# Kernel optimization log

Measured on AMD Instinct MI355X. Metric: run time of the kernel, lower is better.

## Reference

```python
import jax, jax.numpy as jnp
import numpy as np

N = 100000        # nodes
E = 1600000       # edges
F_IN = 128        # input features
H = 64            # hidden
B = 256           # graphs in batch
MIN_SCORE = 1e-3  # SAGPooling min_score
TOL = 1e-7        # PyG topk tolerance
NEG = jnp.float32(-1e30)


def setup_inputs() -> dict:
    key = jax.random.key(0)
    ks = jax.random.split(key, 24)
    x = jax.random.normal(ks[0], (N, F_IN), jnp.float32)
    src = jax.random.randint(ks[1], (E,), 0, N, dtype=jnp.int32)
    dst = jax.random.randint(ks[2], (E,), 0, N, dtype=jnp.int32)
    batch = jnp.sort(jax.random.randint(ks[3], (N,), 0, B, dtype=jnp.int32))
    node_attention = jax.random.uniform(ks[4], (N,), jnp.float32)

    def lin(k, i, o):
        return jax.random.normal(k, (i, o), jnp.float32) / np.float32(np.sqrt(i))

    p = {
        'W11': lin(ks[5], F_IN, H), 'b11': jnp.zeros((H,), jnp.float32),
        'W12': lin(ks[6], H, H),    'b12': jnp.zeros((H,), jnp.float32),
        'gW1': lin(ks[7], H, 1),    'gb1': jnp.zeros((1,), jnp.float32),
        'W21': lin(ks[8], H, H),    'b21': jnp.zeros((H,), jnp.float32),
        'W22': lin(ks[9], H, H),    'b22': jnp.zeros((H,), jnp.float32),
        'gW2': lin(ks[10], H, 1),   'gb2': jnp.zeros((1,), jnp.float32),
        'W31': lin(ks[11], H, H),   'b31': jnp.zeros((H,), jnp.float32),
        'W32': lin(ks[12], H, H),   'b32': jnp.zeros((H,), jnp.float32),
        'Wl':  lin(ks[13], H, 1),   'bl': jnp.zeros((1,), jnp.float32),
    }
    return dict(x=x, src=src, dst=dst, batch=batch, node_attention=node_attention, **p)


def gin_conv(x, src, dst, emask, W1, b1, W2, b2):
    # GINConv, eps=0: mlp(x + sum_{j in N(i)} x_j), edges masked by emask
    agg = jax.ops.segment_sum(x[src] * emask[:, None], dst, num_segments=N)
    h = x + agg
    return jax.nn.relu(h @ W1 + b1) @ W2 + b2


def gcn_attn(x, src, dst, emask, nmask, W, b):
    # GCNConv(H,1) with self-loops + symmetric normalization on the masked graph
    h = x @ W  # [N,1]
    deg = jax.ops.segment_sum(emask, dst, num_segments=N) + nmask
    dinv = jnp.where(deg > 0, jax.lax.rsqrt(jnp.maximum(deg, 1e-12)), 0.0)
    coef = dinv[src] * dinv[dst] * emask
    out = jax.ops.segment_sum(h[src] * coef[:, None], dst, num_segments=N)
    out = out + h * (dinv * dinv * nmask)[:, None] + b
    return out[:, 0]


def seg_softmax(a, batch, nmask):
    am = jnp.where(nmask > 0, a, NEG)
    m = jax.ops.segment_max(am, batch, num_segments=B)
    e = jnp.where(nmask > 0, jnp.exp(a - m[batch]), 0.0)
    s = jax.ops.segment_sum(e, batch, num_segments=B)
    return e / jnp.maximum(s[batch], 1e-30)


def sag_pool(x, src, dst, emask, nmask, batch, W, b):
    attn = gcn_attn(x, src, dst, emask, nmask, W, b)
    score = seg_softmax(attn, batch, nmask)
    smax = jax.ops.segment_max(jnp.where(nmask > 0, score, NEG), batch, num_segments=B)
    thr = jnp.minimum(MIN_SCORE, smax[batch] - TOL)
    keep = ((nmask > 0) & (score > thr)).astype(x.dtype)
    x2 = x * (score * keep)[:, None]          # x[perm] * score[perm], masked form
    emask2 = emask * keep[src] * keep[dst]    # filter_adj
    return x2, emask2, keep, score


def reference(x, src, dst, batch, node_attention,
              W11, b11, W12, b12, gW1, gb1,
              W21, b21, W22, b22, gW2, gb2,
              W31, b31, W32, b32, Wl, bl):
    emask = jnp.ones((E,), x.dtype)
    nmask0 = jnp.ones((N,), x.dtype)

    h = jax.nn.relu(gin_conv(x, src, dst, emask, W11, b11, W12, b12))
    h, emask, keep1, _ = sag_pool(h, src, dst, emask, nmask0, batch, gW1, gb1)

    h = jax.nn.relu(gin_conv(h, src, dst, emask, W21, b21, W22, b22))
    h, emask, keep2, score2 = sag_pool(h, src, dst, emask, keep1, batch, gW2, gb2)

    ratio = jnp.sum(keep2) / jnp.float32(N)

    h = jax.nn.relu(gin_conv(h, src, dst, emask, W31, b31, W32, b32))

    # global max pool over surviving nodes
    hm = jnp.where(keep2[:, None] > 0, h, NEG)
    g = jax.ops.segment_max(hm, batch, num_segments=B)
    out = g @ Wl + bl  # [B,1]

    # attention KL loss; perm2 indexes the pool1-compacted array (as in the source)
    r1 = jnp.clip(jnp.cumsum(keep1).astype(jnp.int32) - 1, 0, N - 1)
    t = node_attention[r1]
    logp = jnp.log(score2 + 1e-14)
    kl = jnp.where(t > 0, t * jnp.log(jnp.maximum(t, 1e-38)), 0.0) - t * logp
    kl = kl * keep2
    s = jax.ops.segment_sum(kl, batch, num_segments=B)
    c = jax.ops.segment_sum(keep2, batch, num_segments=B)
    attn_loss = s / jnp.maximum(c, 1.0)  # scatter_mean

    return out, attn_loss, ratio
```

## Files before the change

### kernel.cpp

```cpp
#include <hip/hip_runtime.h>
#include <hip/hip_fp16.h>
#include <math.h>

#define NN 100000
#define NE 1600000
#define NB 256
#define NEGF (-1e30f)
#define NSCAN_BLK ((NN + 1023) / 1024)
#define GVB 1024
#define P_SORT 256
#define NBKT 391
#define HLEN (NBKT * P_SORT)
#define HSCAN_BLK ((HLEN + 1023) / 1024)
#define BKT_CAP 6144
#define NMASKW 1566

__global__ void k_hist_coarse(const int* __restrict__ dst, const int* __restrict__ batch,
                              int* __restrict__ offs, int* __restrict__ H) {
    __shared__ int lh[NBKT];
    int p = blockIdx.x, tid = threadIdx.x;
    if (p == 0) {
        for (int g = tid; g <= NB; g += 256) {
            int lo = 0, hi = NN;
            while (lo < hi) { int mid = (lo + hi) >> 1; if (batch[mid] < g) lo = mid + 1; else hi = mid; }
            offs[g] = lo;
        }
    }
    for (int i = tid; i < NBKT; i += 256) lh[i] = 0;
    __syncthreads();
    int c0 = p * (NE / P_SORT), c1 = c0 + NE / P_SORT;
    for (int i = c0 + tid; i < c1; i += 256) atomicAdd(&lh[dst[i] >> 8], 1);
    __syncthreads();
    for (int i = tid; i < NBKT; i += 256) H[i * P_SORT + p] = lh[i];
}
__global__ void k_iscan_blk(const int* __restrict__ in, int* __restrict__ pref,
                            int* __restrict__ bsums, int len) {
    int blk = blockIdx.x, tid = threadIdx.x;
    int base = blk * 1024;
    int vals[4], tsum = 0;
    for (int j = 0; j < 4; ++j) {
        int idx = base + tid * 4 + j;
        int v = (idx < len) ? in[idx] : 0;
        vals[j] = tsum; tsum += v;
    }
    __shared__ int sh[256];
    sh[tid] = tsum; __syncthreads();
    for (int o = 1; o < 256; o <<= 1) {
        int v = (tid >= o) ? sh[tid - o] : 0;
        __syncthreads();
        sh[tid] += v;
        __syncthreads();
    }
    int excl = sh[tid] - tsum;
    for (int j = 0; j < 4; ++j) {
        int idx = base + tid * 4 + j;
        if (idx < len) pref[idx] = excl + vals[j];
    }
    if (tid == 255) bsums[blk] = sh[255];
}
__global__ void k_iscan_add(int* __restrict__ pref, const int* __restrict__ bsums, int len) {
    __shared__ int sh[256];
    int t = threadIdx.x;
    int sb = blockIdx.x >> 2;
    sh[t] = (t < sb) ? bsums[t] : 0;
    __syncthreads();
    for (int o = 128; o > 0; o >>= 1) { if (t < o) sh[t] += sh[t + o]; __syncthreads(); }
    int pre = sh[0];
    int idx = blockIdx.x * 256 + t;
    if (idx < len) pref[idx] += pre;
}
__global__ void k_scatter_pairs(const int* __restrict__ src, const int* __restrict__ dst,
                                const int* __restrict__ Hs, int2* __restrict__ ebuf) {
    __shared__ int curs[NBKT];
    int p = blockIdx.x, tid = threadIdx.x;
    for (int i = tid; i < NBKT; i += 256) curs[i] = Hs[i * P_SORT + p];
    __syncthreads();
    int c0 = p * (NE / P_SORT), c1 = c0 + NE / P_SORT;
    for (int i = c0 + tid; i < c1; i += 256) {
        int d = dst[i];
        int pos = atomicAdd(&curs[d >> 8], 1);
        ebuf[pos] = make_int2(src[i], d);
    }
}
__global__ void k_bucket_csr(const int2* __restrict__ ebuf, const int* __restrict__ Hs,
                             int* __restrict__ roffs, int* __restrict__ csrc) {
    __shared__ int hist2[256];
    __shared__ int curs2[256];
    __shared__ int sh[256];
    __shared__ int stage[BKT_CAP];
    int b = blockIdx.x, tid = threadIdx.x;
    int e0 = Hs[b * P_SORT];
    int e1 = (b + 1 < NBKT) ? Hs[(b + 1) * P_SORT] : NE;
    int n0 = b * 256;
    int cntb = e1 - e0;
    if (b == 0 && tid == 0) roffs[NN] = NE;
    hist2[tid] = 0;
    __syncthreads();
    for (int i = e0 + tid; i < e1; i += 256) atomicAdd(&hist2[ebuf[i].y & 255], 1);
    __syncthreads();
    int v = hist2[tid];
    sh[tid] = v; __syncthreads();
    for (int o = 1; o < 256; o <<= 1) {
        int u = (tid >= o) ? sh[tid - o] : 0;
        __syncthreads();
        sh[tid] += u;
        __syncthreads();
    }
    int excl = sh[tid] - v;
    int node = n0 + tid;
    if (node < NN) roffs[node] = e0 + excl;
    curs2[tid] = excl;
    __syncthreads();
    if (cntb <= BKT_CAP) {
        for (int i = e0 + tid; i < e1; i += 256) {
            int2 pr = ebuf[i];
            int pos = atomicAdd(&curs2[pr.y & 255], 1);
            stage[pos] = pr.x;
        }
        __syncthreads();
        for (int i = tid; i < cntb; i += 256) csrc[e0 + i] = stage[i];
    } else {
        for (int i = e0 + tid; i < e1; i += 256) {
            int2 pr = ebuf[i];
            int pos = atomicAdd(&curs2[pr.y & 255], 1);
            csrc[e0 + pos] = pr.x;
        }
    }
}

__global__ __launch_bounds__(256) void k_pre1_g(const float* __restrict__ x,
                                                const float* __restrict__ W,
                                                float* __restrict__ y) {
    __shared__ float lds[4][4 * 128];
    int tid = threadIdx.x, w = tid >> 6, l = tid & 63;
    float Wc[128];
#pragma unroll
    for (int k = 0; k < 128; ++k) Wc[k] = W[k * 64 + l];
    float* row = lds[w];
    int g = blockIdx.x * 4 + w;
    const int G = GVB * 4;
    for (int t = g; t < NN / 4; t += G) {
        int n0 = t * 4;
#pragma unroll
        for (int r = 0; r < 4; ++r) {
            row[r * 128 + l]      = x[(size_t)(n0 + r) * 128 + l];
            row[r * 128 + 64 + l] = x[(size_t)(n0 + r) * 128 + 64 + l];
        }
        __builtin_amdgcn_wave_barrier();
        float acc[4] = {0.f, 0.f, 0.f, 0.f};
#pragma unroll
        for (int k = 0; k < 128; k += 4) {
#pragma unroll
            for (int r = 0; r < 4; ++r) {
                float4 bv = *(const float4*)&row[r * 128 + k];
                acc[r] = fmaf(bv.x, Wc[k],     acc[r]);
                acc[r] = fmaf(bv.y, Wc[k + 1], acc[r]);
                acc[r] = fmaf(bv.z, Wc[k + 2], acc[r]);
                acc[r] = fmaf(bv.w, Wc[k + 3], acc[r]);
            }
        }
        __builtin_amdgcn_wave_barrier();
#pragma unroll
        for (int r = 0; r < 4; ++r) y[(size_t)(n0 + r) * 64 + l] = acc[r];
    }
}

__global__ __launch_bounds__(256) void k_pre23_h(const float* __restrict__ h,
                                                 const float* __restrict__ sk,
                                                 const float* __restrict__ W,
                                                 __half* __restrict__ yh) {
    __shared__ float lds[4][8 * 64];
    int tid = threadIdx.x, w = tid >> 6, l = tid & 63;
    float Wc[64];
#pragma unroll
    for (int k = 0; k < 64; ++k) Wc[k] = W[k * 64 + l];
    float* row = lds[w];
    int g = blockIdx.x * 4 + w;
    const int G = GVB * 4;
    for (int t = g; t < NN / 8; t += G) {
        int n0 = t * 8;
#pragma unroll
        for (int r = 0; r < 8; ++r) row[r * 64 + l] = h[(size_t)(n0 + r) * 64 + l];
        __builtin_amdgcn_wave_barrier();
        float acc[8] = {0.f, 0.f, 0.f, 0.f, 0.f, 0.f, 0.f, 0.f};
#pragma unroll
        for (int k = 0; k < 64; k += 4) {
#pragma unroll
            for (int r = 0; r < 8; ++r) {
                float4 bv = *(const float4*)&row[r * 64 + k];
                acc[r] = fmaf(bv.x, Wc[k],     acc[r]);
                acc[r] = fmaf(bv.y, Wc[k + 1], acc[r]);
                acc[r] = fmaf(bv.z, Wc[k + 2], acc[r]);
                acc[r] = fmaf(bv.w, Wc[k + 3], acc[r]);
            }
        }
        __builtin_amdgcn_wave_barrier();
#pragma unroll
        for (int r = 0; r < 8; ++r)
            yh[(size_t)(n0 + r) * 64 + l] = __float2half(acc[r] * sk[n0 + r]);
    }
}

__global__ __launch_bounds__(256) void k_post_g(const float* __restrict__ zp,
                                                const float* __restrict__ W2,
                                                const float* __restrict__ b2,
                                                const float* __restrict__ gW,
                                                const int* __restrict__ roffs,
                                                const int* __restrict__ cnt,
                                                const float* __restrict__ keep,
                                                float* __restrict__ hOut,
                                                float* __restrict__ hwd,
                                                float* __restrict__ dinv, int mode) {
    __shared__ float lds[4][8 * 64];
    int tid = threadIdx.x, w = tid >> 6, l = tid & 63;
    float Wc[64];
#pragma unroll
    for (int k = 0; k < 64; ++k) Wc[k] = W2[k * 64 + l];
    float b2v = b2[l];
    float gWv = (mode < 3) ? gW[l] : 0.f;
    float* row = lds[w];
    int g = blockIdx.x * 4 + w;
    const int G = GVB * 4;
    for (int t = g; t < NN / 8; t += G) {
        int n0 = t * 8;
#pragma unroll
        for (int r = 0; r < 8; ++r) row[r * 64 + l] = zp[(size_t)(n0 + r) * 64 + l];
        __builtin_amdgcn_wave_barrier();
        float acc[8];
#pragma unroll
        for (int r = 0; r < 8; ++r) acc[r] = b2v;
#pragma unroll
        for (int k = 0; k < 64; k += 4) {
#pragma unroll
            for (int r = 0; r < 8; ++r) {
                float4 bv = *(const float4*)&row[r * 64 + k];
                acc[r] = fmaf(bv.x, Wc[k],     acc[r]);
                acc[r] = fmaf(bv.y, Wc[k + 1], acc[r]);
                acc[r] = fmaf(bv.z, Wc[k + 2], acc[r]);
                acc[r] = fmaf(bv.w, Wc[k + 3], acc[r]);
            }
        }
        __builtin_amdgcn_wave_barrier();
#pragma unroll
        for (int r = 0; r < 8; ++r) {
            acc[r] = fmaxf(acc[r], 0.f);
            hOut[(size_t)(n0 + r) * 64 + l] = acc[r];
        }
        if (mode < 3) {
#pragma unroll
            for (int r = 0; r < 8; ++r) {
                float t2 = acc[r] * gWv;
                for (int o = 32; o > 0; o >>= 1) t2 += __shfl_down(t2, o, 64);
                if (l == 0) {
                    int n = n0 + r;
                    float di;
                    if (mode == 1) di = 1.f / sqrtf((float)(roffs[n + 1] - roffs[n]) + 1.f);
                    else di = (keep[n] != 0.f) ? 1.f / sqrtf((float)cnt[n] + 1.f) : 0.f;
                    dinv[n] = di;
                    hwd[n] = t2 * di;
                }
            }
        }
    }
}

__global__ void k_gather_y(const float* __restrict__ y, const int* __restrict__ roffs,
                           const int* __restrict__ csrc, const float* __restrict__ b1,
                           float* __restrict__ z) {
    int tid = threadIdx.x;
    int d = blockIdx.x * 16 + (tid >> 4);
    int l = tid & 15;
    const float4* y4 = (const float4*)y;
    float4 acc = y4[(size_t)d * 16 + l];
    int e0 = roffs[d], e1 = roffs[d + 1];
    int e = e0;
    for (; e + 3 < e1; e += 4) {
        int s0 = csrc[e], s1 = csrc[e + 1], s2 = csrc[e + 2], s3 = csrc[e + 3];
        float4 v0 = y4[(size_t)s0 * 16 + l];
        float4 v1 = y4[(size_t)s1 * 16 + l];
        float4 v2 = y4[(size_t)s2 * 16 + l];
        float4 v3 = y4[(size_t)s3 * 16 + l];
        acc.x += (v0.x + v1.x) + (v2.x + v3.x);
        acc.y += (v0.y + v1.y) + (v2.y + v3.y);
        acc.z += (v0.z + v1.z) + (v2.z + v3.z);
        acc.w += (v0.w + v1.w) + (v2.w + v3.w);
    }
    for (; e < e1; ++e) {
        float4 v0 = y4[(size_t)csrc[e] * 16 + l];
        acc.x += v0.x; acc.y += v0.y; acc.z += v0.z; acc.w += v0.w;
    }
    float4 o;
    o.x = fmaxf(acc.x + b1[4 * l],     0.f);
    o.y = fmaxf(acc.y + b1[4 * l + 1], 0.f);
    o.z = fmaxf(acc.z + b1[4 * l + 2], 0.f);
    o.w = fmaxf(acc.w + b1[4 * l + 3], 0.f);
    ((float4*)z)[(size_t)d * 16 + l] = o;
}

__global__ void k_gather_h(const __half* __restrict__ yh, const int* __restrict__ roffs,
                           const int* __restrict__ csrc,
                           const unsigned long long* __restrict__ kmask,
                           const float* __restrict__ b1,
                           float* __restrict__ z, int* __restrict__ cnt) {
    int tid = threadIdx.x;
    int d = blockIdx.x * 16 + (tid >> 4);
    int l = tid & 15;
    const float2* yv = (const float2*)yh;
    float2 raw = yv[(size_t)d * 16 + l];
    __half2 p0 = ((const __half2*)&raw)[0], p1 = ((const __half2*)&raw)[1];
    float4 acc = make_float4(__low2float(p0), __high2float(p0),
                             __low2float(p1), __high2float(p1));
    int c = 0;
    if ((kmask[d >> 6] >> (d & 63)) & 1ull) {
        int e0 = roffs[d], e1 = roffs[d + 1];
        int e = e0;
        for (; e + 3 < e1; e += 4) {
            int s0 = csrc[e], s1 = csrc[e + 1], s2 = csrc[e + 2], s3 = csrc[e + 3];
            float2 r0 = yv[(size_t)s0 * 16 + l];
            float2 r1 = yv[(size_t)s1 * 16 + l];
            float2 r2 = yv[(size_t)s2 * 16 + l];
            float2 r3 = yv[(size_t)s3 * 16 + l];
#pragma unroll
            for (int j = 0; j < 4; ++j) {
                float2 rr = (j == 0) ? r0 : (j == 1) ? r1 : (j == 2) ? r2 : r3;
                __half2 a0 = ((const __half2*)&rr)[0], a1 = ((const __half2*)&rr)[1];
                acc.x += __low2float(a0); acc.y += __high2float(a0);
                acc.z += __low2float(a1); acc.w += __high2float(a1);
            }
            if (cnt) c += (int)((kmask[s0 >> 6] >> (s0 & 63)) & 1ull)
                        + (int)((kmask[s1 >> 6] >> (s1 & 63)) & 1ull)
                        + (int)((kmask[s2 >> 6] >> (s2 & 63)) & 1ull)
                        + (int)((kmask[s3 >> 6] >> (s3 & 63)) & 1ull);
        }
        for (; e < e1; ++e) {
            int s0 = csrc[e];
            float2 rr = yv[(size_t)s0 * 16 + l];
            __half2 a0 = ((const __half2*)&rr)[0], a1 = ((const __half2*)&rr)[1];
            acc.x += __low2float(a0); acc.y += __high2float(a0);
            acc.z += __low2float(a1); acc.w += __high2float(a1);
            if (cnt) c += (int)((kmask[s0 >> 6] >> (s0 & 63)) & 1ull);
        }
    }
    float4 o;
    o.x = fmaxf(acc.x + b1[4 * l],     0.f);
    o.y = fmaxf(acc.y + b1[4 * l + 1], 0.f);
    o.z = fmaxf(acc.z + b1[4 * l + 2], 0.f);
    o.w = fmaxf(acc.w + b1[4 * l + 3], 0.f);
    ((float4*)z)[(size_t)d * 16 + l] = o;
    if (cnt && l == 0) cnt[d] = c;
}

__global__ void k_pool(const int* __restrict__ roffs, const int* __restrict__ csrc,
                       const float* __restrict__ hwd, const float* __restrict__ dinv,
                       const float* __restrict__ gb, const float* __restrict__ nmask,
                       const int* __restrict__ offs, float* __restrict__ score,
                       float* __restrict__ keep, float* __restrict__ sk) {
    __shared__ float attn_s[2048];
    __shared__ float red[256];
    int b = blockIdx.x, tid = threadIdx.x;
    int s0 = offs[b], s1 = offs[b + 1];
    int len = s1 - s0;
    float gbv = gb[0];
    for (int j = tid; j < len; j += 256) {
        int i = s0 + j;
        float a = NEGF;
        if (!nmask || nmask[i] > 0.f) {
            float sum = hwd[i];
            int e0 = roffs[i], e1 = roffs[i + 1];
            for (int e = e0; e < e1; ++e) sum += hwd[csrc[e]];
            a = dinv[i] * sum + gbv;
        }
        attn_s[j] = a;
    }
    __syncthreads();
    float m = NEGF;
    for (int j = tid; j < len; j += 256) m = fmaxf(m, attn_s[j]);
    red[tid] = m; __syncthreads();
    for (int o = 128; o > 0; o >>= 1) { if (tid < o) red[tid] = fmaxf(red[tid], red[tid + o]); __syncthreads(); }
    m = red[0]; __syncthreads();
    float s = 0.f;
    for (int j = tid; j < len; j += 256) {
        float a = attn_s[j];
        if (a > 0.5f * NEGF) s += expf(a - m);
    }
    red[tid] = s; __syncthreads();
    for (int o = 128; o > 0; o >>= 1) { if (tid < o) red[tid] += red[tid + o]; __syncthreads(); }
    s = red[0]; __syncthreads();
    float sden = fmaxf(s, 1e-30f);
    float smax = NEGF;
    for (int j = tid; j < len; j += 256) {
        float a = attn_s[j];
        float sc = (a > 0.5f * NEGF) ? expf(a - m) / sden : 0.f;
        score[s0 + j] = sc;
        attn_s[j] = sc;
        smax = fmaxf(smax, (a > 0.5f * NEGF) ? sc : NEGF);
    }
    red[tid] = smax; __syncthreads();
    for (int o = 128; o > 0; o >>= 1) { if (tid < o) red[tid] = fmaxf(red[tid], red[tid + o]); __syncthreads(); }
    smax = red[0]; __syncthreads();
    float thr = fminf(1e-3f, smax - 1e-7f);
    for (int j = tid; j < len; j += 256) {
        float sc = attn_s[j];
        float kp = (sc > thr) ? 1.f : 0.f;
        keep[s0 + j] = kp;
        sk[s0 + j] = sc * kp;
    }
}

__global__ void k_pack(const float* __restrict__ keep, unsigned long long* __restrict__ mask) {
    int i = blockIdx.x * 256 + threadIdx.x;
    float v = (i < NN) ? keep[i] : 0.f;
    unsigned long long m = __ballot(v > 0.f);
    if ((threadIdx.x & 63) == 0) mask[(unsigned)i >> 6] = m;
}

__global__ void k_tail(const float* __restrict__ h, const float* __restrict__ keep2,
                       const int* __restrict__ offs, const float* __restrict__ Wl,
                       const float* __restrict__ bl, const float* __restrict__ score2,
                       const int* __restrict__ prefix, const float* __restrict__ natt,
                       float* __restrict__ out, float* __restrict__ out_loss,
                       float* __restrict__ c_total) {
    int b = blockIdx.x, tid = threadIdx.x;
    int s0 = offs[b], s1 = offs[b + 1];
    int f = tid & 63, g = tid >> 6;
    float m = NEGF;
    for (int i = s0 + g; i < s1; i += 4)
        if (keep2[i] > 0.f) m = fmaxf(m, h[(size_t)i * 64 + f]);
    __shared__ float red[256];
    red[tid] = m; __syncthreads();
    if (g == 0) {
        m = fmaxf(fmaxf(red[f], red[64 + f]), fmaxf(red[128 + f], red[192 + f]));
        float v = m * Wl[f];
        for (int o = 32; o > 0; o >>= 1) v += __shfl_down(v, o, 64);
        if (f == 0) out[b] = v + bl[0];
    }
    __syncthreads();
    float ssum = 0.f, c = 0.f;
    for (int i = s0 + tid; i < s1; i += 256) {
        if (keep2[i] > 0.f) {
            int r1 = prefix[i] - 1;
            r1 = max(0, min(r1, NN - 1));
            float t = natt[r1];
            float logp = logf(score2[i] + 1e-14f);
            float kl = ((t > 0.f) ? t * logf(fmaxf(t, 1e-38f)) : 0.f) - t * logp;
            ssum += kl; c += 1.f;
        }
    }
    __shared__ float rs[256], rc[256];
    rs[tid] = ssum; rc[tid] = c; __syncthreads();
    for (int o = 128; o > 0; o >>= 1) {
        if (tid < o) { rs[tid] += rs[tid + o]; rc[tid] += rc[tid + o]; }
        __syncthreads();
    }
    if (tid == 0) {
        out_loss[b] = rs[0] / fmaxf(rc[0], 1.f);
        atomicAdd(c_total, rc[0]);
    }
}

__global__ void k_scan1(const float* __restrict__ keep1, int* __restrict__ prefix,
                        int* __restrict__ bsums) {
    int blk = blockIdx.x, tid = threadIdx.x;
    int base = blk * 1024;
    int vals[4], tsum = 0;
    for (int j = 0; j < 4; ++j) {
        int idx = base + tid * 4 + j;
        int v = (idx < NN && keep1[idx] > 0.f) ? 1 : 0;
        tsum += v; vals[j] = tsum;
    }
    __shared__ int sh[256];
    sh[tid] = tsum; __syncthreads();
    for (int o = 1; o < 256; o <<= 1) {
        int v = (tid >= o) ? sh[tid - o] : 0;
        __syncthreads();
        sh[tid] += v;
        __syncthreads();
    }
    int excl = sh[tid] - tsum;
    for (int j = 0; j < 4; ++j) {
        int idx = base + tid * 4 + j;
        if (idx < NN) prefix[idx] = excl + vals[j];
    }
    if (tid == 255) bsums[blk] = sh[255];
}
__global__ void k_scan3(int* __restrict__ prefix, const int* __restrict__ bsums) {
    __shared__ int sh[256];
    int t = threadIdx.x;
    int sb = blockIdx.x >> 2;
    sh[t] = (t < sb) ? bsums[t] : 0;
    __syncthreads();
    for (int o = 128; o > 0; o >>= 1) { if (t < o) sh[t] += sh[t + o]; __syncthreads(); }
    int pre = sh[0];
    int idx = blockIdx.x * 256 + t;
    if (idx < NN) prefix[idx] += pre;
}

__global__ void k_final(const float* __restrict__ c_total, float* __restrict__ out) {
    out[0] = c_total[0] / (float)NN;
}

extern "C" void kernel_launch(void* const* d_in, const int* in_sizes, int n_in,
                              void* d_out, int out_size, void* d_ws, size_t ws_size,
                              hipStream_t stream) {
    const float* x    = (const float*)d_in[0];
    const int*   src  = (const int*)d_in[1];
    const int*   dst  = (const int*)d_in[2];
    const int*   batch= (const int*)d_in[3];
    const float* natt = (const float*)d_in[4];
    const float* W11 = (const float*)d_in[5],  *b11 = (const float*)d_in[6];
    const float* W12 = (const float*)d_in[7],  *b12 = (const float*)d_in[8];
    const float* gW1 = (const float*)d_in[9],  *gb1 = (const float*)d_in[10];
    const float* W21 = (const float*)d_in[11], *b21 = (const float*)d_in[12];
    const float* W22 = (const float*)d_in[13], *b22 = (const float*)d_in[14];
    const float* gW2 = (const float*)d_in[15], *gb2 = (const float*)d_in[16];
    const float* W31 = (const float*)d_in[17], *b31 = (const float*)d_in[18];
    const float* W32 = (const float*)d_in[19], *b32 = (const float*)d_in[20];
    const float* Wl  = (const float*)d_in[21], *bl  = (const float*)d_in[22];
    float* out = (float*)d_out;

    float* hA     = (float*)d_ws;
    float* hB     = hA + (size_t)NN * 64;
    float* ybuf   = hB + (size_t)NN * 64;
    float* zbuf   = ybuf + (size_t)NN * 64;
    float* hwd    = zbuf + (size_t)NN * 64;
    float* dinv   = hwd + NN;
    float* score1 = dinv + NN;
    float* keep1  = score1 + NN;
    float* sk1    = keep1 + NN;
    float* score2 = sk1 + NN;
    float* keep2  = score2 + NN;
    float* sk2    = keep2 + NN;
    int*   prefix = (int*)(sk2 + NN);
    int*   cnt    = prefix + NN;
    int*   roffs  = cnt + NN;
    int*   csrc   = roffs + NN + 1;
    int*   offs   = csrc + NE;
    int*   bsums  = offs + NB + 1;
    float* c_total= (float*)(bsums + 128);
    unsigned long long* mask1 = (unsigned long long*)(((uintptr_t)(c_total + 1) + 7) & ~(uintptr_t)7);
    unsigned long long* mask2 = mask1 + NMASKW;
    int*   H      = (int*)ybuf;
    int*   Hs     = H + HLEN;
    int2*  ebuf   = (int2*)zbuf;
    __half* yh    = (__half*)ybuf;

    const int nblk_n   = (NN + 255) / 256;
    const int nblk_n16 = NN / 16;

    k_hist_coarse<<<P_SORT, 256, 0, stream>>>(dst, batch, offs, H);
    k_iscan_blk<<<HSCAN_BLK, 256, 0, stream>>>(H, Hs, bsums, HLEN);
    k_iscan_add<<<(HLEN + 255) / 256, 256, 0, stream>>>(Hs, bsums, HLEN);
    k_scatter_pairs<<<P_SORT, 256, 0, stream>>>(src, dst, Hs, ebuf);
    k_bucket_csr<<<NBKT, 256, 0, stream>>>(ebuf, Hs, roffs, csrc);

    k_pre1_g<<<GVB, 256, 0, stream>>>(x, W11, ybuf);
    k_gather_y<<<nblk_n16, 256, 0, stream>>>(ybuf, roffs, csrc, b11, zbuf);
    k_post_g<<<GVB, 256, 0, stream>>>(zbuf, W12, b12, gW1, roffs, nullptr, nullptr,
                                      hA, hwd, dinv, 1);
    k_pool<<<NB, 256, 0, stream>>>(roffs, csrc, hwd, dinv, gb1, nullptr, offs,
                                   score1, keep1, sk1);
    k_pack<<<nblk_n, 256, 0, stream>>>(keep1, mask1);

    k_pre23_h<<<GVB, 256, 0, stream>>>(hA, sk1, W21, yh);
    k_gather_h<<<nblk_n16, 256, 0, stream>>>(yh, roffs, csrc, mask1, b21, zbuf, cnt);
    k_post_g<<<GVB, 256, 0, stream>>>(zbuf, W22, b22, gW2, roffs, cnt, keep1,
                                      hB, hwd, dinv, 2);
    k_pool<<<NB, 256, 0, stream>>>(roffs, csrc, hwd, dinv, gb2, keep1, offs,
                                   score2, keep2, sk2);
    k_pack<<<nblk_n, 256, 0, stream>>>(keep2, mask2);

    k_pre23_h<<<GVB, 256, 0, stream>>>(hB, sk2, W31, yh);
    k_gather_h<<<nblk_n16, 256, 0, stream>>>(yh, roffs, csrc, mask2, b31, zbuf, nullptr);
    k_post_g<<<GVB, 256, 0, stream>>>(zbuf, W32, b32, nullptr, roffs, nullptr, nullptr,
                                      hA, nullptr, nullptr, 3);

    k_scan1<<<NSCAN_BLK, 256, 0, stream>>>(keep1, prefix, bsums);
    k_scan3<<<nblk_n, 256, 0, stream>>>(prefix, bsums);

    hipMemsetAsync(c_total, 0, sizeof(float), stream);
    k_tail<<<NB, 256, 0, stream>>>(hA, keep2, offs, Wl, bl, score2, prefix, natt,
                                   out, out + NB, c_total);
    k_final<<<1, 1, 0, stream>>>(c_total, out + 2 * NB);
}
```

Measured before the change: 508.0 us.

## Pack edge pairs, widen pool blocks, replace prefix scan with bitmask popcount

Packs each (src, dst-low-byte) edge pair into one 32-bit int, which halves ebuf traffic during the CSR build. k_pool now runs 512 threads per graph. The two-kernel keep1 prefix scan is replaced by a small per-word popcount prefix over mask1, and k_tail computes ranks from it directly. The final ratio kernel is folded into k_tail with a last-block-done counter, so there are fewer launches but one added atomic handshake.

New measurement: 502.1 us. No clear change (-1.2%).

```diff
diff --git a/kernel.cpp b/kernel.cpp
--- a/kernel.cpp
+++ b/kernel.cpp
@@ -6,7 +6,6 @@
 #define NE 1600000
 #define NB 256
 #define NEGF (-1e30f)
-#define NSCAN_BLK ((NN + 1023) / 1024)
 #define GVB 1024
 #define P_SORT 256
 #define NBKT 391
@@ -70,7 +69,7 @@
     if (idx < len) pref[idx] += pre;
 }
 __global__ void k_scatter_pairs(const int* __restrict__ src, const int* __restrict__ dst,
-                                const int* __restrict__ Hs, int2* __restrict__ ebuf) {
+                                const int* __restrict__ Hs, int* __restrict__ ebuf) {
     __shared__ int curs[NBKT];
     int p = blockIdx.x, tid = threadIdx.x;
     for (int i = tid; i < NBKT; i += 256) curs[i] = Hs[i * P_SORT + p];
@@ -79,10 +78,10 @@
     for (int i = c0 + tid; i < c1; i += 256) {
         int d = dst[i];
         int pos = atomicAdd(&curs[d >> 8], 1);
-        ebuf[pos] = make_int2(src[i], d);
-    }
-}
-__global__ void k_bucket_csr(const int2* __restrict__ ebuf, const int* __restrict__ Hs,
+        ebuf[pos] = src[i] | ((d & 255) << 17);
+    }
+}
+__global__ void k_bucket_csr(const int* __restrict__ ebuf, const int* __restrict__ Hs,
                              int* __restrict__ roffs, int* __restrict__ csrc) {
     __shared__ int hist2[256];
     __shared__ int curs2[256];
@@ -96,7 +95,7 @@
     if (b == 0 && tid == 0) roffs[NN] = NE;
     hist2[tid] = 0;
     __syncthreads();
-    for (int i = e0 + tid; i < e1; i += 256) atomicAdd(&hist2[ebuf[i].y & 255], 1);
+    for (int i = e0 + tid; i < e1; i += 256) atomicAdd(&hist2[ebuf[i] >> 17], 1);
     __syncthreads();
     int v = hist2[tid];
     sh[tid] = v; __syncthreads();
@@ -113,17 +112,17 @@
     __syncthreads();
     if (cntb <= BKT_CAP) {
         for (int i = e0 + tid; i < e1; i += 256) {
-            int2 pr = ebuf[i];
-            int pos = atomicAdd(&curs2[pr.y & 255], 1);
-            stage[pos] = pr.x;
+            int pr = ebuf[i];
+            int pos = atomicAdd(&curs2[pr >> 17], 1);
+            stage[pos] = pr & 0x1FFFF;
         }
         __syncthreads();
         for (int i = tid; i < cntb; i += 256) csrc[e0 + i] = stage[i];
     } else {
         for (int i = e0 + tid; i < e1; i += 256) {
-            int2 pr = ebuf[i];
-            int pos = atomicAdd(&curs2[pr.y & 255], 1);
-            csrc[e0 + pos] = pr.x;
+            int pr = ebuf[i];
+            int pos = atomicAdd(&curs2[pr >> 17], 1);
+            csrc[e0 + pos] = pr & 0x1FFFF;
         }
     }
 }
@@ -350,18 +349,19 @@
     if (cnt && l == 0) cnt[d] = c;
 }
 
-__global__ void k_pool(const int* __restrict__ roffs, const int* __restrict__ csrc,
+__global__ __launch_bounds__(512) void k_pool(const int* __restrict__ roffs,
+                       const int* __restrict__ csrc,
                        const float* __restrict__ hwd, const float* __restrict__ dinv,
                        const float* __restrict__ gb, const float* __restrict__ nmask,
                        const int* __restrict__ offs, float* __restrict__ score,
                        float* __restrict__ keep, float* __restrict__ sk) {
     __shared__ float attn_s[2048];
-    __shared__ float red[256];
+    __shared__ float red[512];
     int b = blockIdx.x, tid = threadIdx.x;
     int s0 = offs[b], s1 = offs[b + 1];
     int len = s1 - s0;
     float gbv = gb[0];
-    for (int j = tid; j < len; j += 256) {
+    for (int j = tid; j < len; j += 512) {
         int i = s0 + j;
         float a = NEGF;
         if (!nmask || nmask[i] > 0.f) {
@@ -374,21 +374,21 @@
     }
     __syncthreads();
     float m = NEGF;
-    for (int j = tid; j < len; j += 256) m = fmaxf(m, attn_s[j]);
+    for (int j = tid; j < len; j += 512) m = fmaxf(m, attn_s[j]);
     red[tid] = m; __syncthreads();
-    for (int o = 128; o > 0; o >>= 1) { if (tid < o) red[tid] = fmaxf(red[tid], red[tid + o]); __syncthreads(); }
+    for (int o = 256; o > 0; o >>= 1) { if (tid < o) red[tid] = fmaxf(red[tid], red[tid + o]); __syncthreads(); }
     m = red[0]; __syncthreads();
     float s = 0.f;
-    for (int j = tid; j < len; j += 256) {
+    for (int j = tid; j < len; j += 512) {
         float a = attn_s[j];
         if (a > 0.5f * NEGF) s += expf(a - m);
     }
     red[tid] = s; __syncthreads();
-    for (int o = 128; o > 0; o >>= 1) { if (tid < o) red[tid] += red[tid + o]; __syncthreads(); }
+    for (int o = 256; o > 0; o >>= 1) { if (tid < o) red[tid] += red[tid + o]; __syncthreads(); }
     s = red[0]; __syncthreads();
     float sden = fmaxf(s, 1e-30f);
     float smax = NEGF;
-    for (int j = tid; j < len; j += 256) {
+    for (int j = tid; j < len; j += 512) {
         float a = attn_s[j];
         float sc = (a > 0.5f * NEGF) ? expf(a - m) / sden : 0.f;
         score[s0 + j] = sc;
@@ -396,10 +396,10 @@
         smax = fmaxf(smax, (a > 0.5f * NEGF) ? sc : NEGF);
     }
     red[tid] = smax; __syncthreads();
-    for (int o = 128; o > 0; o >>= 1) { if (tid < o) red[tid] = fmaxf(red[tid], red[tid + o]); __syncthreads(); }
+    for (int o = 256; o > 0; o >>= 1) { if (tid < o) red[tid] = fmaxf(red[tid], red[tid + o]); __syncthreads(); }
     smax = red[0]; __syncthreads();
     float thr = fminf(1e-3f, smax - 1e-7f);
-    for (int j = tid; j < len; j += 256) {
+    for (int j = tid; j < len; j += 512) {
         float sc = attn_s[j];
         float kp = (sc > thr) ? 1.f : 0.f;
         keep[s0 + j] = kp;
@@ -414,12 +414,37 @@
     if ((threadIdx.x & 63) == 0) mask[(unsigned)i >> 6] = m;
 }
 
+__global__ void k_wpref(const unsigned long long* __restrict__ mask, int* __restrict__ wpref) {
+    __shared__ int sh[256];
+    int t = threadIdx.x;
+    int base = t * 7;
+    int cnts[7]; int tsum = 0;
+#pragma unroll
+    for (int j = 0; j < 7; ++j) {
+        int w = base + j;
+        cnts[j] = tsum;
+        if (w < NMASKW) tsum += (int)__popcll(mask[w]);
+    }
+    sh[t] = tsum; __syncthreads();
+    for (int o = 1; o < 256; o <<= 1) {
+        int v = (t >= o) ? sh[t - o] : 0;
+        __syncthreads(); sh[t] += v; __syncthreads();
+    }
+    int excl = sh[t] - tsum;
+#pragma unroll
+    for (int j = 0; j < 7; ++j) {
+        int w = base + j;
+        if (w < NMASKW) wpref[w] = excl + cnts[j];
+    }
+}
+
 __global__ void k_tail(const float* __restrict__ h, const float* __restrict__ keep2,
                        const int* __restrict__ offs, const float* __restrict__ Wl,
                        const float* __restrict__ bl, const float* __restrict__ score2,
-                       const int* __restrict__ prefix, const float* __restrict__ natt,
+                       const unsigned long long* __restrict__ mask1,
+                       const int* __restrict__ wpref, const float* __restrict__ natt,
                        float* __restrict__ out, float* __restrict__ out_loss,
-                       float* __restrict__ c_total) {
+                       float* __restrict__ c_total, int* __restrict__ done) {
     int b = blockIdx.x, tid = threadIdx.x;
     int s0 = offs[b], s1 = offs[b + 1];
     int f = tid & 63, g = tid >> 6;
@@ -438,7 +463,8 @@
     float ssum = 0.f, c = 0.f;
     for (int i = s0 + tid; i < s1; i += 256) {
         if (keep2[i] > 0.f) {
-            int r1 = prefix[i] - 1;
+            int w = i >> 6, bb = i & 63;
+            int r1 = wpref[w] + (int)__popcll(mask1[w] & ((1ull << bb) - 1ull));
             r1 = max(0, min(r1, NN - 1));
             float t = natt[r1];
             float logp = logf(score2[i] + 1e-14f);
@@ -455,48 +481,10 @@
     if (tid == 0) {
         out_loss[b] = rs[0] / fmaxf(rc[0], 1.f);
         atomicAdd(c_total, rc[0]);
-    }
-}
-
-__global__ void k_scan1(const float* __restrict__ keep1, int* __restrict__ prefix,
-                        int* __restrict__ bsums) {
-    int blk = blockIdx.x, tid = threadIdx.x;
-    int base = blk * 1024;
-    int vals[4], tsum = 0;
-    for (int j = 0; j < 4; ++j) {
-        int idx = base + tid * 4 + j;
-        int v = (idx < NN && keep1[idx] > 0.f) ? 1 : 0;
-        tsum += v; vals[j] = tsum;
-    }
-    __shared__ int sh[256];
-    sh[tid] = tsum; __syncthreads();
-    for (int o = 1; o < 256; o <<= 1) {
-        int v = (tid >= o) ? sh[tid - o] : 0;
-        __syncthreads();
-        sh[tid] += v;
-        __syncthreads();
-    }
-    int excl = sh[tid] - tsum;
-    for (int j = 0; j < 4; ++j) {
-        int idx = base + tid * 4 + j;
-        if (idx < NN) prefix[idx] = excl + vals[j];
-    }
-    if (tid == 255) bsums[blk] = sh[255];
-}
-__global__ void k_scan3(int* __restrict__ prefix, const int* __restrict__ bsums) {
-    __shared__ int sh[256];
-    int t = threadIdx.x;
-    int sb = blockIdx.x >> 2;
-    sh[t] = (t < sb) ? bsums[t] : 0;
-    __syncthreads();
-    for (int o = 128; o > 0; o >>= 1) { if (t < o) sh[t] += sh[t + o]; __syncthreads(); }
-    int pre = sh[0];
-    int idx = blockIdx.x * 256 + t;
-    if (idx < NN) prefix[idx] += pre;
-}
-
-__global__ void k_final(const float* __restrict__ c_total, float* __restrict__ out) {
-    out[0] = c_total[0] / (float)NN;
+        __threadfence();
+        int t = atomicAdd(done, 1);
+        if (t == NB - 1) out[2 * NB] = *(volatile float*)c_total / (float)NN;
+    }
 }
 
 extern "C" void kernel_launch(void* const* d_in, const int* in_sizes, int n_in,
@@ -530,18 +518,19 @@
     float* score2 = sk1 + NN;
     float* keep2  = score2 + NN;
     float* sk2    = keep2 + NN;
-    int*   prefix = (int*)(sk2 + NN);
-    int*   cnt    = prefix + NN;
+    int*   wpref  = (int*)(sk2 + NN);
+    int*   cnt    = wpref + NMASKW;
     int*   roffs  = cnt + NN;
     int*   csrc   = roffs + NN + 1;
     int*   offs   = csrc + NE;
     int*   bsums  = offs + NB + 1;
     float* c_total= (float*)(bsums + 128);
-    unsigned long long* mask1 = (unsigned long long*)(((uintptr_t)(c_total + 1) + 7) & ~(uintptr_t)7);
+    int*   done   = (int*)(c_total + 1);
+    unsigned long long* mask1 = (unsigned long long*)(((uintptr_t)(done + 1) + 7) & ~(uintptr_t)7);
     unsigned long long* mask2 = mask1 + NMASKW;
     int*   H      = (int*)ybuf;
     int*   Hs     = H + HLEN;
-    int2*  ebuf   = (int2*)zbuf;
+    int*   ebuf   = (int*)zbuf;
     __half* yh    = (__half*)ybuf;
 
     const int nblk_n   = (NN + 255) / 256;
@@ -557,15 +546,16 @@
     k_gather_y<<<nblk_n16, 256, 0, stream>>>(ybuf, roffs, csrc, b11, zbuf);
     k_post_g<<<GVB, 256, 0, stream>>>(zbuf, W12, b12, gW1, roffs, nullptr, nullptr,
                                       hA, hwd, dinv, 1);
-    k_pool<<<NB, 256, 0, stream>>>(roffs, csrc, hwd, dinv, gb1, nullptr, offs,
+    k_pool<<<NB, 512, 0, stream>>>(roffs, csrc, hwd, dinv, gb1, nullptr, offs,
                                    score1, keep1, sk1);
     k_pack<<<nblk_n, 256, 0, stream>>>(keep1, mask1);
+    k_wpref<<<1, 256, 0, stream>>>(mask1, wpref);
 
     k_pre23_h<<<GVB, 256, 0, stream>>>(hA, sk1, W21, yh);
     k_gather_h<<<nblk_n16, 256, 0, stream>>>(yh, roffs, csrc, mask1, b21, zbuf, cnt);
     k_post_g<<<GVB, 256, 0, stream>>>(zbuf, W22, b22, gW2, roffs, cnt, keep1,
                                       hB, hwd, dinv, 2);
-    k_pool<<<NB, 256, 0, stream>>>(roffs, csrc, hwd, dinv, gb2, keep1, offs,
+    k_pool<<<NB, 512, 0, stream>>>(roffs, csrc, hwd, dinv, gb2, keep1, offs,
                                    score2, keep2, sk2);
     k_pack<<<nblk_n, 256, 0, stream>>>(keep2, mask2);
 
@@ -574,11 +564,7 @@
     k_post_g<<<GVB, 256, 0, stream>>>(zbuf, W32, b32, nullptr, roffs, nullptr, nullptr,
                                       hA, nullptr, nullptr, 3);
 
-    k_scan1<<<NSCAN_BLK, 256, 0, stream>>>(keep1, prefix, bsums);
-    k_scan3<<<nblk_n, 256, 0, stream>>>(prefix, bsums);
-
-    hipMemsetAsync(c_total, 0, sizeof(float), stream);
-    k_tail<<<NB, 256, 0, stream>>>(hA, keep2, offs, Wl, bl, score2, prefix, natt,
-                                   out, out + NB, c_total);
-    k_final<<<1, 1, 0, stream>>>(c_total, out + 2 * NB);
-}
+    hipMemsetAsync(c_total, 0, sizeof(float) + sizeof(int), stream);
+    k_tail<<<NB, 256, 0, stream>>>(hA, keep2, offs, Wl, bl, score2, mask1, wpref, natt,
+                                   out, out + NB, c_total, done);
+}
```
